# Optimization experiments

Hardware: AMD Instinct MI355X
Metric: run time of the kernel (lower is better)

The kernel has to match this reference:

```python
import jax, jax.numpy as jnp
import numpy as np

B, T, E, D = 128, 512, 128, 128

def setup_inputs() -> dict:
    key = jax.random.key(0)
    ks = jax.random.split(key, 20)
    s = 0.05
    return {
        'encoder_states': jax.random.normal(ks[0], (B, T, E), jnp.float32),
        'labels': jax.random.normal(ks[1], (B, T), jnp.float32),
        'init_h': jax.random.normal(ks[2], (B, D), jnp.float32),
        'init_c': jax.random.normal(ks[3], (B, D), jnp.float32),
        'init_ctx': jax.random.normal(ks[4], (B, E), jnp.float32),
        # Attention: W maps concat(h,c) (2D) -> T, U maps E -> T, V maps T -> 1
        'Wa': jax.random.normal(ks[5], (2 * D, T), jnp.float32) * s,
        'ba': jnp.zeros((T,), jnp.float32),
        'Ua': jax.random.normal(ks[6], (E, T), jnp.float32) * s,
        'bu': jnp.zeros((T,), jnp.float32),
        'Va': jax.random.normal(ks[7], (T, 1), jnp.float32) * s,
        'bv': jnp.zeros((1,), jnp.float32),
        # layer_fc_context: (1+E) -> 1
        'Wc': jax.random.normal(ks[8], (1 + E, 1), jnp.float32) * s,
        'bc': jnp.zeros((1,), jnp.float32),
        # LSTMCell: input dim 1, hidden D; gate order i, f, g(candidate), o (Keras)
        'Wk': jax.random.normal(ks[9], (1, 4 * D), jnp.float32) * s,
        'Wr': jax.random.normal(ks[10], (D, 4 * D), jnp.float32) * s,
        'bl': jnp.zeros((4 * D,), jnp.float32),
        # prediction FCs: (D+E)->D, D->1
        'W1': jax.random.normal(ks[11], (D + E, D), jnp.float32) * s,
        'b1': jnp.zeros((D,), jnp.float32),
        'W2': jax.random.normal(ks[12], (D, 1), jnp.float32) * s,
        'b2': jnp.zeros((1,), jnp.float32),
    }


def reference(encoder_states, labels, init_h, init_c, init_ctx,
              Wa, ba, Ua, bu, Va, bv, Wc, bc, Wk, Wr, bl, W1, b1, W2, b2):
    # Loop-invariant attention term U(encoder_states): (B, T, T)
    u_enc = jnp.einsum('bte,tn->btn'[0:14].replace('t','t') if False else 'bte,en->btn', encoder_states, Ua) + bu

    def step(carry, label_t):
        h, c, _ctx = carry
        # additive attention over time axis
        s = jnp.concatenate([h, c], axis=-1) @ Wa + ba            # (B, T)
        e = jnp.tanh(u_enc + s[:, None, :])                        # (B, T, T)
        score = (e @ Va)[..., 0] + bv                              # (B, T)
        w = jax.nn.softmax(score, axis=1)                          # (B, T)
        ctx = jnp.einsum('bt,bte->be', w, encoder_states)          # (B, E)
        # context-gated input
        y = jnp.concatenate([label_t[:, None], ctx], axis=-1) @ Wc + bc   # (B, 1)
        # Keras LSTMCell step
        z = y @ Wk + h @ Wr + bl                                   # (B, 4D)
        i, f, g, o = jnp.split(z, 4, axis=-1)
        c_new = jax.nn.sigmoid(f) * c + jax.nn.sigmoid(i) * jnp.tanh(g)
        h_new = jax.nn.sigmoid(o) * jnp.tanh(c_new)
        return (h_new, c_new, ctx), None

    (h, c, ctx), _ = jax.lax.scan(step, (init_h, init_c, init_ctx), labels.T)
    pred = (jnp.concatenate([h, ctx], axis=-1) @ W1 + b1) @ W2 + b2   # (B, 1)
    return pred
```

## Files before the change

kernel.cpp:

```cpp
#include <hip/hip_runtime.h>
#include <hip/hip_fp16.h>

#define B_ 128
#define T_ 512
#define E_ 128
#define D_ 128

#define C2f 2.885390081777927f
#define L2E 1.4426950408889634f

__device__ __forceinline__ float rcpf_(float x){ return __builtin_amdgcn_rcpf(x); }
__device__ __forceinline__ float ex2_(float x){ return __builtin_amdgcn_exp2f(x); }

__device__ __forceinline__ void gstoref(float* p, float v){
    __hip_atomic_store(p, v, __ATOMIC_RELAXED, __HIP_MEMORY_SCOPE_AGENT);
}
__device__ __forceinline__ float gloadf(const float* p){
    return __hip_atomic_load(p, __ATOMIC_RELAXED, __HIP_MEMORY_SCOPE_AGENT);
}
__device__ __forceinline__ void flag_set(int* p, int v){
    __hip_atomic_store(p, v, __ATOMIC_RELEASE, __HIP_MEMORY_SCOPE_AGENT);
}
__device__ __forceinline__ void flag_wait(int* p, int v){
    int it = 0;
    while (__hip_atomic_load(p, __ATOMIC_ACQUIRE, __HIP_MEMORY_SCOPE_AGENT) < v
           && it < (1 << 26)){ it++; __builtin_amdgcn_s_sleep(2); }
}

__global__ __launch_bounds__(256) void transpose_half(const float* __restrict__ in,
                                                      __half* __restrict__ out,
                                                      int K, int N){
    __shared__ float tile[32][33];
    int n0 = blockIdx.x * 32, k0 = blockIdx.y * 32;
    int tx = threadIdx.x & 31, ty = threadIdx.x >> 5;
    #pragma unroll
    for (int i = ty; i < 32; i += 8)
        tile[i][tx] = in[(size_t)(k0 + i) * N + n0 + tx];
    __syncthreads();
    #pragma unroll
    for (int i = ty; i < 32; i += 8)
        out[(size_t)(n0 + i) * K + k0 + tx] = __float2half(tile[tx][i]);
}

__global__ __launch_bounds__(512) void g_kernel(const float* __restrict__ enc,
                                                const float* __restrict__ Wc,
                                                float* __restrict__ g){
    int b = blockIdx.x, t = threadIdx.x;
    const float4* ep = (const float4*)(enc + ((size_t)b * T_ + t) * E_);
    float acc = 0.f;
    #pragma unroll
    for (int i = 0; i < 32; i++){
        float4 ev = ep[i];
        acc = fmaf(ev.x, Wc[1 + 4*i + 0], acc);
        acc = fmaf(ev.y, Wc[1 + 4*i + 1], acc);
        acc = fmaf(ev.z, Wc[1 + 4*i + 2], acc);
        acc = fmaf(ev.w, Wc[1 + 4*i + 3], acc);
    }
    g[(size_t)b * T_ + t] = acc;
}

__global__ __launch_bounds__(256) void uenc_kernel(const float* __restrict__ enc,
                                                   const float* __restrict__ Ua,
                                                   const float* __restrict__ bu,
                                                   __half* __restrict__ P){
    int b = blockIdx.z;
    int t0 = blockIdx.x * 64;
    int n0 = blockIdx.y * 64;
    int tt = threadIdx.x & 63;
    int ng = threadIdx.x >> 6;
    const float* erow = enc + ((size_t)b * T_ + (t0 + tt)) * E_;
    const float* uap  = Ua + n0 + ng * 16;
    float acc[16];
    #pragma unroll
    for (int i = 0; i < 16; i++) acc[i] = 0.f;
    #pragma unroll 2
    for (int e0 = 0; e0 < E_; e0 += 4){
        float4 av = *(const float4*)(erow + e0);
        #pragma unroll
        for (int ee = 0; ee < 4; ee++){
            float a = (ee==0)?av.x:(ee==1)?av.y:(ee==2)?av.z:av.w;
            const float4* u4 = (const float4*)(uap + (size_t)(e0+ee) * T_);
            float4 x0 = u4[0], x1 = u4[1], x2 = u4[2], x3 = u4[3];
            acc[0]  = fmaf(a, x0.x, acc[0]);  acc[1]  = fmaf(a, x0.y, acc[1]);
            acc[2]  = fmaf(a, x0.z, acc[2]);  acc[3]  = fmaf(a, x0.w, acc[3]);
            acc[4]  = fmaf(a, x1.x, acc[4]);  acc[5]  = fmaf(a, x1.y, acc[5]);
            acc[6]  = fmaf(a, x1.z, acc[6]);  acc[7]  = fmaf(a, x1.w, acc[7]);
            acc[8]  = fmaf(a, x2.x, acc[8]);  acc[9]  = fmaf(a, x2.y, acc[9]);
            acc[10] = fmaf(a, x2.z, acc[10]); acc[11] = fmaf(a, x2.w, acc[11]);
            acc[12] = fmaf(a, x3.x, acc[12]); acc[13] = fmaf(a, x3.y, acc[13]);
            acc[14] = fmaf(a, x3.z, acc[14]); acc[15] = fmaf(a, x3.w, acc[15]);
        }
    }
    int nb = n0 + ng * 16;
    #pragma unroll
    for (int i = 0; i < 16; i++){
        float u = acc[i] + bu[nb + i];
        P[(size_t)b * T_ * T_ + (size_t)(nb + i) * T_ + t0 + tt] = __float2half(ex2_(C2f * u));
    }
}

__device__ __forceinline__ void dot8(float& acc, uint4 wv, float4 ha, float4 hb){
    float2 f0 = __half22float2(*reinterpret_cast<__half2*>(&wv.x));
    float2 f1 = __half22float2(*reinterpret_cast<__half2*>(&wv.y));
    float2 f2 = __half22float2(*reinterpret_cast<__half2*>(&wv.z));
    float2 f3 = __half22float2(*reinterpret_cast<__half2*>(&wv.w));
    acc = fmaf(ha.x, f0.x, acc); acc = fmaf(ha.y, f0.y, acc);
    acc = fmaf(ha.z, f1.x, acc); acc = fmaf(ha.w, f1.y, acc);
    acc = fmaf(hb.x, f2.x, acc); acc = fmaf(hb.y, f2.y, acc);
    acc = fmaf(hb.z, f3.x, acc); acc = fmaf(hb.w, f3.y, acc);
}

__device__ __forceinline__ void acc8(uint4 pv, float2 qv,
    float& a0, float& a1, float& a2, float& a3,
    float& a4, float& a5, float& a6, float& a7)
{
    float2 f0 = __half22float2(*reinterpret_cast<__half2*>(&pv.x));
    float2 f1 = __half22float2(*reinterpret_cast<__half2*>(&pv.y));
    float2 f2 = __half22float2(*reinterpret_cast<__half2*>(&pv.z));
    float2 f3 = __half22float2(*reinterpret_cast<__half2*>(&pv.w));
    float m;
    m = fmaf(f0.x, qv.x, 1.f); a0 = fmaf(rcpf_(m), qv.y, a0);
    m = fmaf(f0.y, qv.x, 1.f); a1 = fmaf(rcpf_(m), qv.y, a1);
    m = fmaf(f1.x, qv.x, 1.f); a2 = fmaf(rcpf_(m), qv.y, a2);
    m = fmaf(f1.y, qv.x, 1.f); a3 = fmaf(rcpf_(m), qv.y, a3);
    m = fmaf(f2.x, qv.x, 1.f); a4 = fmaf(rcpf_(m), qv.y, a4);
    m = fmaf(f2.y, qv.x, 1.f); a5 = fmaf(rcpf_(m), qv.y, a5);
    m = fmaf(f3.x, qv.x, 1.f); a6 = fmaf(rcpf_(m), qv.y, a6);
    m = fmaf(f3.y, qv.x, 1.f); a7 = fmaf(rcpf_(m), qv.y, a7);
}

__global__ __launch_bounds__(1024) void decoder_kernel(
    const float* __restrict__ enc,
    const float* __restrict__ labels,
    const float* __restrict__ init_h, const float* __restrict__ init_c,
    const float* __restrict__ Va,
    const float* __restrict__ ba, const float* __restrict__ bl,
    const float* __restrict__ Wc, const float* __restrict__ bc,
    const float* __restrict__ Wk,
    const float* __restrict__ W1, const float* __restrict__ b1,
    const float* __restrict__ W2, const float* __restrict__ b2,
    const __half* __restrict__ Wa_t, const __half* __restrict__ Wr_t,
    const __half* __restrict__ Pw, const float* __restrict__ gbuf,
    float* __restrict__ psbuf, int* __restrict__ fA,
    float* __restrict__ out)
{
    __shared__ __align__(16) __half Plds[128 * 512];
    __shared__ __align__(16) float hc_s[256];
    __shared__ __align__(16) float ctx_s[128];
    __shared__ __align__(16) float Q_s[256];
    __shared__ __align__(16) float Vam_s[256];
    __shared__ __align__(16) float sc[512];
    __shared__ __align__(16) float rz_s[512];
    __shared__ __align__(16) float g_s[512];
    __shared__ __align__(16) float scratch[4096];
    __shared__ __align__(16) float ba_s[256], bl_s[256];
    __shared__ __align__(16) float Wk_s[512];
    __shared__ float Wc_s[132];
    __shared__ float red[20];

    const int tid = threadIdx.x;
    const int b = blockIdx.x;
    const int h_ = blockIdx.y;
    const int par_stride = B_ * 2;

    if (tid < 128){
        hc_s[tid]       = init_h[b*128 + tid];
        hc_s[128 + tid] = init_c[b*128 + tid];
    }
    if (tid < 256){
        Vam_s[tid] = -2.f * Va[256*h_ + tid];
        ba_s[tid]  = ba[256*h_ + tid];
        bl_s[tid]  = bl[256*h_ + tid];
    }
    if (tid < 512){
        Wk_s[tid] = Wk[tid];
        g_s[tid]  = gbuf[(size_t)b * T_ + tid];
    }
    if (tid < 129) Wc_s[tid] = Wc[tid];
    if (tid == 129) Wc_s[130] = bc[0];

    const __half* Pb  = Pw + ((size_t)b * T_ + 256 * h_) * T_;
    const uint4*  Pb4 = (const uint4*)Pb;

    {
        int wid = tid >> 6, lane = tid & 63;
        for (int r = wid; r < 128; r += 16){
            int g = r >> 3, j = r & 7;
            *((uint4*)Plds + (size_t)r * 64 + lane) =
                Pb4[(size_t)(16*g + j) * 64 + lane];
        }
    }
    __syncthreads();

    int* myfA = &fA[b*2 + h_];   int* pfA = &fA[b*2 + (1 - h_)];

    const int np_ = tid & 255;
    const int kq_ = tid >> 8;

    for (int t = 0; t < T_; t++){
        const int par = t & 1;
        float* psme = psbuf + ((size_t)par * par_stride + b*2 + h_)     * 768;
        float* pspr = psbuf + ((size_t)par * par_stride + b*2 + (1-h_)) * 768;

        {
            const float4* hc4 = (const float4*)hc_s;
            {
                float acc = (kq_ == 0) ? ba_s[np_] : 0.f;
                const uint4* wa = (const uint4*)(Wa_t + (size_t)(256*h_ + np_) * 256 + kq_ * 64);
                #pragma unroll 4
                for (int i = 0; i < 8; i++){
                    uint4 wv = wa[i];
                    dot8(acc, wv, hc4[kq_*16 + 2*i], hc4[kq_*16 + 2*i + 1]);
                }
                scratch[kq_*256 + np_] = acc;
            }
            {
                float accr = (kq_ == 0) ? bl_s[np_] : 0.f;
                const uint4* wr = (const uint4*)(Wr_t + (size_t)(256*h_ + np_) * 128 + kq_ * 32);
                #pragma unroll
                for (int i = 0; i < 4; i++){
                    uint4 wv = wr[i];
                    dot8(accr, wv, hc4[kq_*8 + 2*i], hc4[kq_*8 + 2*i + 1]);
                }
                scratch[1024 + kq_*256 + np_] = accr;
            }
        }
        __syncthreads();
        if (tid < 256){
            float s = scratch[tid] + scratch[256+tid] + scratch[512+tid] + scratch[768+tid];
            Q_s[tid] = ex2_(C2f * s);
        } else if (tid < 512){
            int m = tid - 256;
            float rzv = scratch[1024+m] + scratch[1280+m] + scratch[1536+m] + scratch[1792+m];
            rz_s[256*h_ + m] = rzv;
            gstoref(&psme[512 + m], rzv);
        }
        __syncthreads();

        float a0=0.f,a1=0.f,a2=0.f,a3=0.f,a4=0.f,a5=0.f,a6=0.f,a7=0.f;
        {
            int q = tid & 63, g = tid >> 6;
            const uint4* Pl = (const uint4*)Plds + (size_t)(8*g) * 64 + q;
            #pragma unroll
            for (int j = 0; j < 8; j++){
                uint4 pv = Pl[j * 64];
                float2 qv = make_float2(Q_s[16*g + j], Vam_s[16*g + j]);
                acc8(pv, qv, a0,a1,a2,a3,a4,a5,a6,a7);
            }
            const uint4* Pg = Pb4 + (size_t)(16*g + 8) * 64 + q;
            #pragma unroll 4
            for (int j = 0; j < 8; j++){
                uint4 pv = Pg[(size_t)j * 64];
                float2 qv = make_float2(Q_s[16*g + 8 + j], Vam_s[16*g + 8 + j]);
                acc8(pv, qv, a0,a1,a2,a3,a4,a5,a6,a7);
            }
        }
        {
            int q = tid & 63, g = tid >> 6;
            float4* o = (float4*)(scratch + (g & 7)*512 + q*8);
            if (g >= 8){
                o[0] = make_float4(a0,a1,a2,a3);
                o[1] = make_float4(a4,a5,a6,a7);
            }
            __syncthreads();
            if (g < 8){
                float4 p0 = o[0], p1 = o[1];
                o[0] = make_float4(a0+p0.x, a1+p0.y, a2+p0.z, a3+p0.w);
                o[1] = make_float4(a4+p1.x, a5+p1.y, a6+p1.z, a7+p1.w);
            }
        }
        __syncthreads();
        if (tid < 512){
            float v = 0.f;
            #pragma unroll
            for (int g = 0; g < 8; g++) v += scratch[g*512 + tid];
            sc[tid] = v;
            gstoref(&psme[tid], v);
        }
        __syncthreads();
        if (tid == 0){ flag_set(myfA, t + 1); flag_wait(pfA, t + 1); }
        __syncthreads();
        if (tid < 512){
            float score = sc[tid] + gloadf(&pspr[tid]);
            float p = ex2_(score * L2E);
            sc[tid] = p;
            float ss = p;
            float sg = p * g_s[tid];
            #pragma unroll
            for (int off = 32; off; off >>= 1){
                ss += __shfl_xor(ss, off);
                sg += __shfl_xor(sg, off);
            }
            if ((tid & 63) == 0){ red[tid >> 6] = ss; red[8 + (tid >> 6)] = sg; }
        } else if (tid < 768){
            int m = tid - 512;
            rz_s[256*(1-h_) + m] = gloadf(&pspr[512 + m]);
        }
        __syncthreads();

        if (tid < 128){
            float dn = red[0]+red[1]+red[2]+red[3]+red[4]+red[5]+red[6]+red[7];
            float pg = red[8]+red[9]+red[10]+red[11]+red[12]+red[13]+red[14]+red[15];
            float lab = labels[(size_t)b * T_ + t];
            float y = fmaf(lab, Wc_s[0], pg * rcpf_(dn) + Wc_s[130]);
            float zi = rz_s[tid]       + y * Wk_s[tid];
            float zf = rz_s[128 + tid] + y * Wk_s[128 + tid];
            float zg = rz_s[256 + tid] + y * Wk_s[256 + tid];
            float zo = rz_s[384 + tid] + y * Wk_s[384 + tid];
            float si = rcpf_(1.f + ex2_(-L2E * zi));
            float sf = rcpf_(1.f + ex2_(-L2E * zf));
            float so = rcpf_(1.f + ex2_(-L2E * zo));
            float tg_ = 1.f - 2.f * rcpf_(ex2_(C2f * zg) + 1.f);
            float cn = sf * hc_s[128 + tid] + si * tg_;
            float tc = 1.f - 2.f * rcpf_(ex2_(C2f * cn) + 1.f);
            hc_s[128 + tid] = cn;
            hc_s[tid] = so * tc;
        }
        __syncthreads();
    }

    {
        int eq = tid & 31, tg = tid >> 5;
        float4 acc = make_float4(0.f,0.f,0.f,0.f);
        const float4* ep = (const float4*)(enc + ((size_t)b*T_ + tg*16)*E_) + eq;
        #pragma unroll
        for (int i = 0; i < 16; i++){
            float w = sc[tg*16 + i];
            float4 ev = ep[(size_t)i * 32];
            acc.x = fmaf(w, ev.x, acc.x); acc.y = fmaf(w, ev.y, acc.y);
            acc.z = fmaf(w, ev.z, acc.z); acc.w = fmaf(w, ev.w, acc.w);
        }
        *(float4*)(scratch + tg*128 + eq*4) = acc;
    }
    __syncthreads();
    if (tid < 128){
        float s = 0.f;
        #pragma unroll
        for (int g2 = 0; g2 < 32; g2++) s += scratch[g2*128 + tid];
        float dn = red[0]+red[1]+red[2]+red[3]+red[4]+red[5]+red[6]+red[7];
        ctx_s[tid] = s * rcpf_(dn);
    }
    __syncthreads();

    if (tid < 128){
        float acc = b1[tid];
        for (int k = 0; k < 128; k++) acc = fmaf(hc_s[k],  W1[k*128 + tid], acc);
        for (int k = 0; k < 128; k++) acc = fmaf(ctx_s[k], W1[(128+k)*128 + tid], acc);
        scratch[tid] = acc * W2[tid];
    }
    __syncthreads();
    if (h_ == 0 && tid < 64){
        float a = scratch[tid] + scratch[64 + tid];
        #pragma unroll
        for (int off = 32; off; off >>= 1) a += __shfl_xor(a, off);
        if (tid == 0) out[b] = a + b2[0];
    }
}

extern "C" void kernel_launch(void* const* d_in, const int* in_sizes, int n_in,
                              void* d_out, int out_size, void* d_ws, size_t ws_size,
                              hipStream_t stream){
    const float* enc      = (const float*)d_in[0];
    const float* labels   = (const float*)d_in[1];
    const float* init_h   = (const float*)d_in[2];
    const float* init_c   = (const float*)d_in[3];
    const float* Wa = (const float*)d_in[5];
    const float* ba = (const float*)d_in[6];
    const float* Ua = (const float*)d_in[7];
    const float* bu = (const float*)d_in[8];
    const float* Va = (const float*)d_in[9];
    const float* Wc = (const float*)d_in[11];
    const float* bc = (const float*)d_in[12];
    const float* Wk = (const float*)d_in[13];
    const float* Wr = (const float*)d_in[14];
    const float* bl = (const float*)d_in[15];
    const float* W1 = (const float*)d_in[16];
    const float* b1 = (const float*)d_in[17];
    const float* W2 = (const float*)d_in[18];
    const float* b2 = (const float*)d_in[19];

    char* ws = (char*)d_ws;
    const size_t szP = (size_t)B_ * T_ * T_ * 2;
    const size_t szWa = 512 * 256 * 2;
    const size_t szWr = 512 * 128 * 2;
    const size_t szG  = (size_t)B_ * T_ * 4;

    __half* P    = (__half*)ws;
    __half* Wa_t = (__half*)(ws + szP);
    __half* Wr_t = (__half*)(ws + szP + szWa);
    float*  gbuf = (float*)(ws + szP + szWa + szWr);
    float* psbuf = (float*)(ws + szP + szWa + szWr + szG);
    int*   flags = (int*)(psbuf + 2*256*768);

    hipMemsetAsync(flags, 0, 512 * sizeof(int), stream);

    transpose_half<<<dim3(16, 8, 1), 256, 0, stream>>>(Wa, Wa_t, 256, 512);
    transpose_half<<<dim3(16, 4, 1), 256, 0, stream>>>(Wr, Wr_t, 128, 512);
    g_kernel<<<B_, 512, 0, stream>>>(enc, Wc, gbuf);

    dim3 g1(T_/64, T_/64, B_);
    uenc_kernel<<<g1, 256, 0, stream>>>(enc, Ua, bu, P);

    decoder_kernel<<<dim3(B_, 2), 1024, 0, stream>>>(enc,
        labels, init_h, init_c, Va, ba, bl, Wc, bc, Wk, W1, b1, W2, b2,
        Wa_t, Wr_t, P, gbuf, psbuf, flags, (float*)d_out);
}
```

Before: 7.541 ms.

## Reduce gate matvec partials with wave shuffles and wait on flags per wave

The Wa/Wr matvec mapping changes so that four adjacent lanes split the K dimension of one output row. Their partial sums are combined with xor shuffles instead of being written to LDS scratch and summed after two block barriers. Because each wave now produces exactly the Q_s entries it later reads in the P accumulation, the block-wide barrier before that phase can be dropped. The cross-block flag wait moves from thread 0 plus a __syncthreads to lane 0 of each consuming wave, removing another barrier per timestep. The biases move into registers, which costs a little extra register pressure, and correctness now relies on the within-wave LDS ordering and on a per-wave acquire.

```diff
diff --git a/kernel.cpp b/kernel.cpp
--- a/kernel.cpp
+++ b/kernel.cpp
@@ -153,7 +153,6 @@
     __shared__ __align__(16) float rz_s[512];
     __shared__ __align__(16) float g_s[512];
     __shared__ __align__(16) float scratch[4096];
-    __shared__ __align__(16) float ba_s[256], bl_s[256];
     __shared__ __align__(16) float Wk_s[512];
     __shared__ float Wc_s[132];
     __shared__ float red[20];
@@ -163,15 +162,15 @@
     const int h_ = blockIdx.y;
     const int par_stride = B_ * 2;
 
+    const int lane = tid & 63, wid = tid >> 6;
+    const int rowA = (wid << 4) + (lane >> 2);
+    const int kqA  = lane & 3;
+
     if (tid < 128){
         hc_s[tid]       = init_h[b*128 + tid];
         hc_s[128 + tid] = init_c[b*128 + tid];
     }
-    if (tid < 256){
-        Vam_s[tid] = -2.f * Va[256*h_ + tid];
-        ba_s[tid]  = ba[256*h_ + tid];
-        bl_s[tid]  = bl[256*h_ + tid];
-    }
+    if (tid < 256) Vam_s[tid] = -2.f * Va[256*h_ + tid];
     if (tid < 512){
         Wk_s[tid] = Wk[tid];
         g_s[tid]  = gbuf[(size_t)b * T_ + tid];
@@ -179,11 +178,13 @@
     if (tid < 129) Wc_s[tid] = Wc[tid];
     if (tid == 129) Wc_s[130] = bc[0];
 
+    const float ba_reg = ba[256*h_ + rowA];
+    const float bl_reg = bl[256*h_ + rowA];
+
     const __half* Pb  = Pw + ((size_t)b * T_ + 256 * h_) * T_;
     const uint4*  Pb4 = (const uint4*)Pb;
 
     {
-        int wid = tid >> 6, lane = tid & 63;
         for (int r = wid; r < 128; r += 16){
             int g = r >> 3, j = r & 7;
             *((uint4*)Plds + (size_t)r * 64 + lane) =
@@ -194,8 +195,8 @@
 
     int* myfA = &fA[b*2 + h_];   int* pfA = &fA[b*2 + (1 - h_)];
 
-    const int np_ = tid & 255;
-    const int kq_ = tid >> 8;
+    const uint4* waA = (const uint4*)(Wa_t + (size_t)(256*h_ + rowA) * 256 + kqA * 64);
+    const uint4* wrA = (const uint4*)(Wr_t + (size_t)(256*h_ + rowA) * 128 + kqA * 32);
 
     for (int t = 0; t < T_; t++){
         const int par = t & 1;
@@ -204,42 +205,31 @@
 
         {
             const float4* hc4 = (const float4*)hc_s;
-            {
-                float acc = (kq_ == 0) ? ba_s[np_] : 0.f;
-                const uint4* wa = (const uint4*)(Wa_t + (size_t)(256*h_ + np_) * 256 + kq_ * 64);
-                #pragma unroll 4
-                for (int i = 0; i < 8; i++){
-                    uint4 wv = wa[i];
-                    dot8(acc, wv, hc4[kq_*16 + 2*i], hc4[kq_*16 + 2*i + 1]);
-                }
-                scratch[kq_*256 + np_] = acc;
-            }
-            {
-                float accr = (kq_ == 0) ? bl_s[np_] : 0.f;
-                const uint4* wr = (const uint4*)(Wr_t + (size_t)(256*h_ + np_) * 128 + kq_ * 32);
-                #pragma unroll
-                for (int i = 0; i < 4; i++){
-                    uint4 wv = wr[i];
-                    dot8(accr, wv, hc4[kq_*8 + 2*i], hc4[kq_*8 + 2*i + 1]);
-                }
-                scratch[1024 + kq_*256 + np_] = accr;
-            }
-        }
-        __syncthreads();
-        if (tid < 256){
-            float s = scratch[tid] + scratch[256+tid] + scratch[512+tid] + scratch[768+tid];
-            Q_s[tid] = ex2_(C2f * s);
-        } else if (tid < 512){
-            int m = tid - 256;
-            float rzv = scratch[1024+m] + scratch[1280+m] + scratch[1536+m] + scratch[1792+m];
-            rz_s[256*h_ + m] = rzv;
-            gstoref(&psme[512 + m], rzv);
-        }
-        __syncthreads();
+            float s = 0.f, r = 0.f;
+            #pragma unroll 4
+            for (int i = 0; i < 8; i++){
+                uint4 wv = waA[i];
+                dot8(s, wv, hc4[kqA*16 + 2*i], hc4[kqA*16 + 2*i + 1]);
+            }
+            #pragma unroll
+            for (int i = 0; i < 4; i++){
+                uint4 wv = wrA[i];
+                dot8(r, wv, hc4[kqA*8 + 2*i], hc4[kqA*8 + 2*i + 1]);
+            }
+            s += __shfl_xor(s, 1); s += __shfl_xor(s, 2);
+            r += __shfl_xor(r, 1); r += __shfl_xor(r, 2);
+            if (kqA == 0){
+                Q_s[rowA] = ex2_(C2f * (s + ba_reg));
+            } else if (kqA == 1){
+                float rzv = r + bl_reg;
+                rz_s[256*h_ + rowA] = rzv;
+                gstoref(&psme[512 + rowA], rzv);
+            }
+        }
 
         float a0=0.f,a1=0.f,a2=0.f,a3=0.f,a4=0.f,a5=0.f,a6=0.f,a7=0.f;
         {
-            int q = tid & 63, g = tid >> 6;
+            int q = lane, g = wid;
             const uint4* Pl = (const uint4*)Plds + (size_t)(8*g) * 64 + q;
             #pragma unroll
             for (int j = 0; j < 8; j++){
@@ -256,7 +246,7 @@
             }
         }
         {
-            int q = tid & 63, g = tid >> 6;
+            int q = lane, g = wid;
             float4* o = (float4*)(scratch + (g & 7)*512 + q*8);
             if (g >= 8){
                 o[0] = make_float4(a0,a1,a2,a3);
@@ -278,8 +268,8 @@
             gstoref(&psme[tid], v);
         }
         __syncthreads();
-        if (tid == 0){ flag_set(myfA, t + 1); flag_wait(pfA, t + 1); }
-        __syncthreads();
+        if (tid == 0) flag_set(myfA, t + 1);
+        if ((tid & 63) == 0 && tid < 768) flag_wait(pfA, t + 1);
         if (tid < 512){
             float score = sc[tid] + gloadf(&pspr[tid]);
             float p = ex2_(score * L2E);
```

New measurement: 23.02 ms. 3.05x slower.
